# Kernel tuning notes

Measured on AMD Instinct MI355X. Metric: run time of the kernel, lower is better.

The kernel has to match this reference:

```python
import jax, jax.numpy as jnp
import numpy as np

NEG_SLOPE = 0.05

def _leaky(v):
    return jnp.where(v >= 0, v, NEG_SLOPE * v)

def setup_inputs() -> dict:
    key = jax.random.key(0)
    ks = jax.random.split(key, 9)
    B, N, D = 8, 96, 16
    H0, H1, OUT = 50, 50, 64
    x = jax.random.normal(ks[0], (B, N, D), dtype=jnp.float32)
    # dense 0/1 adjacency (float, used directly in matmuls), avg degree ~ 0.15*N
    adj = (jax.random.uniform(ks[1], (B, N, N)) < 0.15).astype(jnp.float32)
    h1 = 3 * D + 3          # 51
    h2 = 2 * D + H0 + 1     # 83
    h3 = D + H1             # 66
    W1 = jax.random.normal(ks[2], (h1, H0), dtype=jnp.float32) / np.sqrt(h1)
    b1 = jax.random.normal(ks[3], (H0,), dtype=jnp.float32) * 0.01
    W2 = jax.random.normal(ks[4], (h2, H1), dtype=jnp.float32) / np.sqrt(h2)
    b2 = jax.random.normal(ks[5], (H1,), dtype=jnp.float32) * 0.01
    W3 = jax.random.normal(ks[6], (h3, OUT), dtype=jnp.float32) / np.sqrt(h3)
    b3 = jax.random.normal(ks[7], (OUT,), dtype=jnp.float32) * 0.01
    return {"x": x, "adj": adj, "W1": W1, "b1": b1, "W2": W2, "b2": b2, "W3": W3, "b3": b3}

def reference(x, adj, W1, b1, W2, b2, W3, b3):
    # Faithful math of SpatialGraphConv.forward, with the O(N^4)/O(N^3)
    # broadcast+concat+GEMM algebraically decomposed into O(N^2) einsums
    # (identical result: the concat-GEMM is a sum of per-block contributions).
    B, N, D = x.shape
    H0 = W1.shape[1]
    # pairwise distances dis[b,i,j]
    diff = x[:, :, None, :] - x[:, None, :, :]            # (B,N,N,D)
    dis = jnp.sqrt(jnp.sum(diff * diff, axis=-1) + 1e-10)  # (B,N,N)
    # split W1 rows per concat block [x_i | x_j | x_k | d_ij | d_jk | d_ik]
    Wxi, Wxj, Wxk = W1[:D], W1[D:2 * D], W1[2 * D:3 * D]
    w_ij, w_jk, w_ik = W1[3 * D], W1[3 * D + 1], W1[3 * D + 2]  # (H0,)
    A = x @ Wxi   # (B,N,H0), indexed by i
    Bm = x @ Wxj  # (B,N,H0), indexed by j
    C = x @ Wxk   # (B,N,H0), indexed by k
    # m3_sum[b,i,j,h] = adj[b,i,j] * sum_k adj[b,j,k] * m3pre[b,i,j,k,h]
    deg = jnp.sum(adj, axis=-1)                           # (B,N): sum_k adj[b,j,k]
    sumC = jnp.einsum('bjk,bkh->bjh', adj, C)             # (B,N,H0)
    sd_jk = jnp.sum(adj * dis, axis=-1)                   # (B,N): sum_k adj[j,k]*dis[j,k]
    sd_ik = jnp.einsum('bik,bjk->bij', dis, adj)          # (B,N,N): sum_k adj[j,k]*dis[i,k]
    S = (deg[:, None, :, None] * (A[:, :, None, :] + Bm[:, None, :, :] + b1
                                   + dis[..., None] * w_ij)
         + sumC[:, None, :, :]
         + sd_jk[:, None, :, None] * w_jk
         + sd_ik[..., None] * w_ik)                        # (B,N,N,H0)
    m3_sum = _leaky(adj[..., None] * S)                    # (B,N,N,H0)
    # stage 2: pairwise concat [x_i | x_j | dis | m3_sum] -> MLP -> adj-masked sum over j
    xi = jnp.broadcast_to(x[:, :, None, :], (B, N, N, D))
    xj = jnp.broadcast_to(x[:, None, :, :], (B, N, N, D))
    feat2 = jnp.concatenate([xi, xj, dis[..., None], m3_sum], axis=-1)  # (B,N,N,2D+1+H0)
    m2 = feat2 @ W2 + b2                                   # (B,N,N,H1)
    m2_sum = _leaky(jnp.einsum('bijh,bij->bih', m2, adj))  # (B,N,H1)
    # stage 3: node-wise MLP
    m1 = _leaky(jnp.concatenate([x, m2_sum], axis=-1) @ W3 + b3)  # (B,N,OUT)
    return m1
```

## Files before the change

### kernel.cpp

```cpp
#include <hip/hip_runtime.h>
#include <math.h>

#define BB   8
#define NN   96
#define DD   16
#define H0D  50
#define H1D  50
#define OUTD 64
#define XP   17

typedef unsigned long long u64;


__device__ __forceinline__ float wave_reduce_sum(float v) {
    #pragma unroll
    for (int off = 1; off < 64; off <<= 1)
        v += __shfl_xor(v, off, 64);
    return v;
}

__global__ __launch_bounds__(64) void kA(
    const float* __restrict__ x, const float* __restrict__ adj,
    const float* __restrict__ W1,
    float* __restrict__ disws, u64* __restrict__ maskws,
    float* __restrict__ degws, float* __restrict__ sdjkws,
    float* __restrict__ nxws, float* __restrict__ APws)
{
    const int b = blockIdx.x / NN, j = blockIdx.x % NN;
    const int lane = threadIdx.x;
    __shared__ float sx[NN * XP];
    __shared__ float snx[DD];

    const float4* x4 = (const float4*)(x + (size_t)b * NN * DD);
    #pragma unroll
    for (int t = lane; t < NN * DD / 4; t += 64) {
        float4 v = x4[t];
        int row = t >> 2, d = (t & 3) * 4;
        float* p = &sx[row * XP + d];
        p[0] = v.x; p[1] = v.y; p[2] = v.z; p[3] = v.w;
    }
    const float* arow = adj + ((size_t)b * NN + j) * NN;
    float a0 = arow[lane];
    float a1 = (lane < NN - 64) ? arow[64 + lane] : 0.f;
    u64 m0 = __ballot(a0 != 0.f);
    u64 m1 = __ballot(a1 != 0.f);
    __syncthreads();

    const float* xj = &sx[j * XP];
    float d0, d1 = 0.f;
    {
        float s = 1e-10f;
        const float* xk = &sx[lane * XP];
        #pragma unroll
        for (int d = 0; d < DD; ++d) { float t = xj[d] - xk[d]; s += t * t; }
        d0 = sqrtf(s);
    }
    if (lane < NN - 64) {
        float s = 1e-10f;
        const float* xk = &sx[(64 + lane) * XP];
        #pragma unroll
        for (int d = 0; d < DD; ++d) { float t = xj[d] - xk[d]; s += t * t; }
        d1 = sqrtf(s);
    }
    float* drow = disws + ((size_t)b * NN + j) * NN;
    drow[lane] = d0;
    if (lane < NN - 64) drow[64 + lane] = d1;

    float deg = (float)(__popcll(m0) + __popcll(m1));
    float part = (((m0 >> lane) & 1) ? d0 : 0.f)
               + ((lane < 32 && ((m1 >> lane) & 1)) ? d1 : 0.f);
    float sdjk = wave_reduce_sum(part);
    if (lane == 0) {
        degws[b * NN + j]  = deg;
        sdjkws[b * NN + j] = sdjk;
        maskws[(b * NN + j) * 2 + 0] = m0;
        maskws[(b * NN + j) * 2 + 1] = m1;
    }

    {
        int c = lane >> 4, d = lane & 15;
        unsigned sm;
        if (c == 0)      sm = (unsigned)(m0 & 0xFFFFFFu);
        else if (c == 1) sm = (unsigned)((m0 >> 24) & 0xFFFFFFu);
        else if (c == 2) sm = (unsigned)((m0 >> 48) & 0xFFFFu) | ((unsigned)(m1 & 0xFFu) << 16);
        else             sm = (unsigned)((m1 >> 8) & 0xFFFFFFu);
        float s = 0.f;
        int base = c * 24;
        while (sm) {
            int k = base + __ffs(sm) - 1;
            sm &= sm - 1;
            s += sx[k * XP + d];
        }
        s += __shfl_xor(s, 16, 64);
        s += __shfl_xor(s, 32, 64);
        if (lane < DD) {
            snx[lane] = s;
            nxws[(b * NN + j) * DD + lane] = s;
        }
    }
    __syncthreads();

    if (lane < H0D) {
        float a = 0.f, bm = 0.f, sc = 0.f;
        #pragma unroll
        for (int d = 0; d < DD; ++d) {
            float xv = xj[d];
            a  += xv * W1[d * H0D + lane];
            bm += xv * W1[(DD + d) * H0D + lane];
            sc += snx[d] * W1[(2 * DD + d) * H0D + lane];
        }
        float* ap = APws + ((size_t)b * NN + j) * 128;
        ap[lane]      = a;
        ap[64 + lane] = deg * bm + sc;
    }
}

__global__ __launch_bounds__(64) void kB(
    const float* __restrict__ x,
    const float* __restrict__ W1, const float* __restrict__ b1,
    const float* __restrict__ W2, const float* __restrict__ b2,
    const float* __restrict__ W3, const float* __restrict__ b3,
    const float* __restrict__ disws, const u64* __restrict__ maskws,
    const float* __restrict__ degws, const float* __restrict__ sdjkws,
    const float* __restrict__ nxws, const float* __restrict__ APws,
    float* __restrict__ out)
{
    const int b = blockIdx.x / NN, i = blockIdx.x % NN;
    const int lane = threadIdx.x;
    __shared__ u64 sm0[NN], sm1[NN];
    __shared__ float sdis[NN], sdeg[NN], ssdjk[NN], ssdik[NN];
    __shared__ float smsum[H0D], sm2[H1D], sxi[DD], snxi[DD];

    const ulonglong2* mp = (const ulonglong2*)(maskws + (size_t)b * NN * 2);
    #pragma unroll
    for (int t = lane; t < NN; t += 64) {
        ulonglong2 m = mp[t];
        sm0[t] = m.x; sm1[t] = m.y;
    }
    const float* drow = disws + ((size_t)b * NN + i) * NN;
    sdis[lane] = drow[lane];
    if (lane < 32) sdis[64 + lane] = drow[64 + lane];
    sdeg[lane] = degws[b * NN + lane];
    if (lane < 32) sdeg[64 + lane] = degws[b * NN + 64 + lane];
    ssdjk[lane] = sdjkws[b * NN + lane];
    if (lane < 32) ssdjk[64 + lane] = sdjkws[b * NN + 64 + lane];
    if (lane < DD) {
        sxi[lane]  = x[((size_t)b * NN + i) * DD + lane];
        snxi[lane] = nxws[(b * NN + i) * DD + lane];
    }
    __syncthreads();

    {
        u64 mm0 = sm0[lane], mm1 = sm1[lane];
        float s = 0.f;
        while (mm0) { int k = __ffsll(mm0) - 1;      mm0 &= mm0 - 1; s += sdis[k]; }
        while (mm1) { int k = 64 + __ffsll(mm1) - 1; mm1 &= mm1 - 1; s += sdis[k]; }
        ssdik[lane] = s;
        if (lane < 32) {
            int j = 64 + lane;
            u64 n0 = sm0[j], n1 = sm1[j];
            float t = 0.f;
            while (n0) { int k = __ffsll(n0) - 1;      n0 &= n0 - 1; t += sdis[k]; }
            while (n1) { int k = 64 + __ffsll(n1) - 1; n1 &= n1 - 1; t += sdis[k]; }
            ssdik[j] = t;
        }
    }
    __syncthreads();

    {
        const int h = (lane < H0D) ? lane : 0;
        float ab  = APws[((size_t)b * NN + i) * 128 + h] + b1[h];
        float wij = W1[(3 * DD + 0) * H0D + h];
        float wjk = W1[(3 * DD + 1) * H0D + h];
        float wik = W1[(3 * DD + 2) * H0D + h];
        float msum = 0.f;
        u64 mm = sm0[i]; int base = 0;
        for (int half = 0; half < 2; ++half) {
            while (mm) {
                int j = base + __ffsll(mm) - 1;
                mm &= mm - 1;
                float S = sdeg[j] * (ab + sdis[j] * wij)
                        + APws[((size_t)b * NN + j) * 128 + 64 + h]
                        + ssdjk[j] * wjk + ssdik[j] * wik;
                msum += (S >= 0.f) ? S : 0.05f * S;
            }
            mm = sm1[i]; base = 64;
        }
        if (lane < H0D) smsum[lane] = msum;
    }
    __syncthreads();

    const float degi = sdeg[i], sdjki = ssdjk[i];
    if (lane < H1D) {
        float s = degi * b2[lane];
        #pragma unroll
        for (int d = 0; d < DD; ++d)
            s += degi * sxi[d] * W2[d * H1D + lane]
               + snxi[d] * W2[(DD + d) * H1D + lane];
        s += sdjki * W2[(2 * DD) * H1D + lane];
        for (int c = 0; c < H0D; ++c)
            s += smsum[c] * W2[(2 * DD + 1 + c) * H1D + lane];
        sm2[lane] = (s >= 0.f) ? s : 0.05f * s;
    }
    __syncthreads();

    {
        float s = b3[lane];
        #pragma unroll
        for (int d = 0; d < DD; ++d) s += sxi[d] * W3[d * OUTD + lane];
        for (int h = 0; h < H1D; ++h) s += sm2[h] * W3[(DD + h) * OUTD + lane];
        s = (s >= 0.f) ? s : 0.05f * s;
        out[((size_t)b * NN + i) * OUTD + lane] = s;
    }
}

extern "C" void kernel_launch(void* const* d_in, const int* in_sizes, int n_in,
                              void* d_out, int out_size, void* d_ws, size_t ws_size,
                              hipStream_t stream) {
    const float* x   = (const float*)d_in[0];
    const float* adj = (const float*)d_in[1];
    const float* W1  = (const float*)d_in[2];
    const float* b1  = (const float*)d_in[3];
    const float* W2  = (const float*)d_in[4];
    const float* b2  = (const float*)d_in[5];
    const float* W3  = (const float*)d_in[6];
    const float* b3  = (const float*)d_in[7];
    float* out = (float*)d_out;

    u64*   maskws = (u64*)d_ws;
    float* fbase  = (float*)((char*)d_ws + BB * NN * 2 * sizeof(u64));
    float* disws  = fbase;
    float* degws  = disws + BB * NN * NN;
    float* sdjkws = degws + BB * NN;
    float* nxws   = sdjkws + BB * NN;
    float* APws   = nxws + BB * NN * DD;

    kA<<<BB * NN, 64, 0, stream>>>(x, adj, W1, disws, maskws, degws, sdjkws, nxws, APws);
    kB<<<BB * NN, 64, 0, stream>>>(x, W1, b1, W2, b2, W3, b3,
                                   disws, maskws, degws, sdjkws, nxws, APws, out);
}
```

Before: 83.96 us.

## Fuse both kernels into one per-node block with recomputed neighbor stats

Replaces the two-kernel pipeline (per-node precompute to global workspace, then per-node aggregation) with a single 256-thread kernel per (batch, node i). Each block recomputes the quantities it needs for each neighbor j (adjacency mask, degree, distance sums, neighbor-feature sums, projected W1 terms), with 4 waves splitting the neighbors. This removes the second launch and the global workspace round trip. The cost is redundant recomputation of per-j data across every block that has j as a neighbor, plus more LDS per block.

```diff
diff --git a/kernel.cpp b/kernel.cpp
--- a/kernel.cpp
+++ b/kernel.cpp
@@ -12,205 +12,204 @@
 typedef unsigned long long u64;
 
 
-__device__ __forceinline__ float wave_reduce_sum(float v) {
-    #pragma unroll
-    for (int off = 1; off < 64; off <<= 1)
-        v += __shfl_xor(v, off, 64);
-    return v;
-}
-
-__global__ __launch_bounds__(64) void kA(
+__global__ __launch_bounds__(256) void sgc_one(
     const float* __restrict__ x, const float* __restrict__ adj,
-    const float* __restrict__ W1,
-    float* __restrict__ disws, u64* __restrict__ maskws,
-    float* __restrict__ degws, float* __restrict__ sdjkws,
-    float* __restrict__ nxws, float* __restrict__ APws)
+    const float* __restrict__ W1, const float* __restrict__ b1,
+    const float* __restrict__ W2, const float* __restrict__ b2,
+    const float* __restrict__ W3, const float* __restrict__ b3,
+    float* __restrict__ out)
 {
-    const int b = blockIdx.x / NN, j = blockIdx.x % NN;
-    const int lane = threadIdx.x;
+    const int b = blockIdx.x / NN, i = blockIdx.x % NN;
+    const int tid = threadIdx.x, wv = tid >> 6, lane = tid & 63;
+
     __shared__ float sx[NN * XP];
-    __shared__ float snx[DD];
+    __shared__ float sdisI[NN];
+    __shared__ int   nbrs[NN];
+    __shared__ int   scnt;
+    __shared__ u64   smi[2];
+    __shared__ float sA[H0D];
+    __shared__ float sP[NN * H0D];
+    __shared__ float sdegc[NN], ssdjkc[NN], ssdikc[NN];
+    __shared__ float pmsum[4 * 64];
+    __shared__ float smsum[H0D];
+    __shared__ float sm2[H1D];
+    __shared__ float snxi[DD];
+    __shared__ float sdegi, ssdjki;
 
     const float4* x4 = (const float4*)(x + (size_t)b * NN * DD);
-    #pragma unroll
-    for (int t = lane; t < NN * DD / 4; t += 64) {
+    for (int t = tid; t < NN * DD / 4; t += 256) {
         float4 v = x4[t];
         int row = t >> 2, d = (t & 3) * 4;
         float* p = &sx[row * XP + d];
         p[0] = v.x; p[1] = v.y; p[2] = v.z; p[3] = v.w;
     }
-    const float* arow = adj + ((size_t)b * NN + j) * NN;
-    float a0 = arow[lane];
-    float a1 = (lane < NN - 64) ? arow[64 + lane] : 0.f;
-    u64 m0 = __ballot(a0 != 0.f);
-    u64 m1 = __ballot(a1 != 0.f);
-    __syncthreads();
-
-    const float* xj = &sx[j * XP];
-    float d0, d1 = 0.f;
+    if (wv == 0) {
+        const float* arow = adj + ((size_t)b * NN + i) * NN;
+        u64 m0 = __ballot(arow[lane] != 0.f);
+        float a1 = (lane < 32) ? arow[64 + lane] : 0.f;
+        u64 m1 = __ballot(a1 != 0.f);
+        int c0 = __popcll(m0);
+        if ((m0 >> lane) & 1)
+            nbrs[__popcll(m0 & ((1ull << lane) - 1))] = lane;
+        if (lane < 32 && ((m1 >> lane) & 1))
+            nbrs[c0 + __popcll(m1 & ((1ull << lane) - 1))] = 64 + lane;
+        if (lane == 0) {
+            int c = c0 + __popcll(m1);
+            scnt = c;
+            smi[0] = m0; smi[1] = m1;
+            sdegi = (float)c;
+        }
+    }
+    __syncthreads();
+
+    if (tid < NN) {
+        const float* xi = &sx[i * XP];
+        const float* xk = &sx[tid * XP];
+        float s = 1e-10f;
+        #pragma unroll
+        for (int d = 0; d < DD; ++d) { float t = xi[d] - xk[d]; s += t * t; }
+        sdisI[tid] = sqrtf(s);
+    } else if (tid < NN + H0D) {
+        int h = tid - NN;
+        float s = 0.f;
+        #pragma unroll
+        for (int d = 0; d < DD; ++d) s += sx[i * XP + d] * W1[d * H0D + h];
+        sA[h] = s;
+    }
+    __syncthreads();
+
+    const int cnt = scnt;
     {
-        float s = 1e-10f;
-        const float* xk = &sx[lane * XP];
-        #pragma unroll
-        for (int d = 0; d < DD; ++d) { float t = xj[d] - xk[d]; s += t * t; }
-        d0 = sqrtf(s);
-    }
-    if (lane < NN - 64) {
-        float s = 1e-10f;
-        const float* xk = &sx[(64 + lane) * XP];
-        #pragma unroll
-        for (int d = 0; d < DD; ++d) { float t = xj[d] - xk[d]; s += t * t; }
-        d1 = sqrtf(s);
-    }
-    float* drow = disws + ((size_t)b * NN + j) * NN;
-    drow[lane] = d0;
-    if (lane < NN - 64) drow[64 + lane] = d1;
-
-    float deg = (float)(__popcll(m0) + __popcll(m1));
-    float part = (((m0 >> lane) & 1) ? d0 : 0.f)
-               + ((lane < 32 && ((m1 >> lane) & 1)) ? d1 : 0.f);
-    float sdjk = wave_reduce_sum(part);
-    if (lane == 0) {
-        degws[b * NN + j]  = deg;
-        sdjkws[b * NN + j] = sdjk;
-        maskws[(b * NN + j) * 2 + 0] = m0;
-        maskws[(b * NN + j) * 2 + 1] = m1;
-    }
+        const int hl = (lane < H0D) ? lane : H0D - 1;
+        float wxj[DD], wxk[DD];
+        #pragma unroll
+        for (int d = 0; d < DD; ++d) {
+            wxj[d] = W1[(DD + d) * H0D + hl];
+            wxk[d] = W1[(2 * DD + d) * H0D + hl];
+        }
+        const int ch = lane >> 4, dd = lane & 15;
+        for (int c = wv; c < cnt; c += 4) {
+            const int j = nbrs[c];
+            const float* arow = adj + ((size_t)b * NN + j) * NN;
+            u64 mj0 = __ballot(arow[lane] != 0.f);
+            float a1 = (lane < 32) ? arow[64 + lane] : 0.f;
+            u64 mj1 = __ballot(a1 != 0.f);
+            float deg = (float)(__popcll(mj0) + __popcll(mj1));
+            const float* xj = &sx[j * XP];
+            float d0, d1 = 0.f;
+            {
+                float s = 1e-10f;
+                const float* xk = &sx[lane * XP];
+                #pragma unroll
+                for (int d = 0; d < DD; ++d) { float t = xj[d] - xk[d]; s += t * t; }
+                d0 = sqrtf(s);
+            }
+            if (lane < 32) {
+                float s = 1e-10f;
+                const float* xk = &sx[(64 + lane) * XP];
+                #pragma unroll
+                for (int d = 0; d < DD; ++d) { float t = xj[d] - xk[d]; s += t * t; }
+                d1 = sqrtf(s);
+            }
+            float p1 = ((mj0 >> lane) & 1) ? d0 : 0.f;
+            float p2 = ((mj0 >> lane) & 1) ? sdisI[lane] : 0.f;
+            if (lane < 32 && ((mj1 >> lane) & 1)) { p1 += d1; p2 += sdisI[64 + lane]; }
+            #pragma unroll
+            for (int off = 1; off < 64; off <<= 1) {
+                p1 += __shfl_xor(p1, off, 64);
+                p2 += __shfl_xor(p2, off, 64);
+            }
+            unsigned sm;
+            if (ch == 0)      sm = (unsigned)(mj0 & 0xFFFFFFu);
+            else if (ch == 1) sm = (unsigned)((mj0 >> 24) & 0xFFFFFFu);
+            else if (ch == 2) sm = (unsigned)((mj0 >> 48) & 0xFFFFu) | ((unsigned)(mj1 & 0xFFu) << 16);
+            else              sm = (unsigned)((mj1 >> 8) & 0xFFFFFFu);
+            float nxv = 0.f;
+            const int base = ch * 24;
+            while (sm) {
+                int k = base + __ffs(sm) - 1;
+                sm &= sm - 1;
+                nxv += sx[k * XP + dd];
+            }
+            nxv += __shfl_xor(nxv, 16, 64);
+            nxv += __shfl_xor(nxv, 32, 64);
+            float bm = 0.f, sc = 0.f;
+            #pragma unroll
+            for (int d = 0; d < DD; ++d) {
+                bm += xj[d] * wxj[d];
+                sc += __shfl(nxv, d, 64) * wxk[d];
+            }
+            if (lane < H0D) sP[c * H0D + lane] = deg * bm + sc;
+            if (lane == 0) { sdegc[c] = deg; ssdjkc[c] = p1; ssdikc[c] = p2; }
+        }
+        if (wv == 0) {
+            u64 mi0 = smi[0], mi1 = smi[1];
+            float p = ((mi0 >> lane) & 1) ? sdisI[lane] : 0.f;
+            if (lane < 32 && ((mi1 >> lane) & 1)) p += sdisI[64 + lane];
+            #pragma unroll
+            for (int off = 1; off < 64; off <<= 1) p += __shfl_xor(p, off, 64);
+            if (lane == 0) ssdjki = p;
+            unsigned sm;
+            if (ch == 0)      sm = (unsigned)(mi0 & 0xFFFFFFu);
+            else if (ch == 1) sm = (unsigned)((mi0 >> 24) & 0xFFFFFFu);
+            else if (ch == 2) sm = (unsigned)((mi0 >> 48) & 0xFFFFu) | ((unsigned)(mi1 & 0xFFu) << 16);
+            else              sm = (unsigned)((mi1 >> 8) & 0xFFFFFFu);
+            float nxv = 0.f;
+            const int base = ch * 24;
+            while (sm) {
+                int k = base + __ffs(sm) - 1;
+                sm &= sm - 1;
+                nxv += sx[k * XP + dd];
+            }
+            nxv += __shfl_xor(nxv, 16, 64);
+            nxv += __shfl_xor(nxv, 32, 64);
+            if (lane < DD) snxi[lane] = nxv;
+        }
+    }
+    __syncthreads();
 
     {
-        int c = lane >> 4, d = lane & 15;
-        unsigned sm;
-        if (c == 0)      sm = (unsigned)(m0 & 0xFFFFFFu);
-        else if (c == 1) sm = (unsigned)((m0 >> 24) & 0xFFFFFFu);
-        else if (c == 2) sm = (unsigned)((m0 >> 48) & 0xFFFFu) | ((unsigned)(m1 & 0xFFu) << 16);
-        else             sm = (unsigned)((m1 >> 8) & 0xFFFFFFu);
-        float s = 0.f;
-        int base = c * 24;
-        while (sm) {
-            int k = base + __ffs(sm) - 1;
-            sm &= sm - 1;
-            s += sx[k * XP + d];
-        }
-        s += __shfl_xor(s, 16, 64);
-        s += __shfl_xor(s, 32, 64);
-        if (lane < DD) {
-            snx[lane] = s;
-            nxws[(b * NN + j) * DD + lane] = s;
-        }
-    }
-    __syncthreads();
-
-    if (lane < H0D) {
-        float a = 0.f, bm = 0.f, sc = 0.f;
-        #pragma unroll
-        for (int d = 0; d < DD; ++d) {
-            float xv = xj[d];
-            a  += xv * W1[d * H0D + lane];
-            bm += xv * W1[(DD + d) * H0D + lane];
-            sc += snx[d] * W1[(2 * DD + d) * H0D + lane];
-        }
-        float* ap = APws + ((size_t)b * NN + j) * 128;
-        ap[lane]      = a;
-        ap[64 + lane] = deg * bm + sc;
-    }
-}
-
-__global__ __launch_bounds__(64) void kB(
-    const float* __restrict__ x,
-    const float* __restrict__ W1, const float* __restrict__ b1,
-    const float* __restrict__ W2, const float* __restrict__ b2,
-    const float* __restrict__ W3, const float* __restrict__ b3,
-    const float* __restrict__ disws, const u64* __restrict__ maskws,
-    const float* __restrict__ degws, const float* __restrict__ sdjkws,
-    const float* __restrict__ nxws, const float* __restrict__ APws,
-    float* __restrict__ out)
-{
-    const int b = blockIdx.x / NN, i = blockIdx.x % NN;
-    const int lane = threadIdx.x;
-    __shared__ u64 sm0[NN], sm1[NN];
-    __shared__ float sdis[NN], sdeg[NN], ssdjk[NN], ssdik[NN];
-    __shared__ float smsum[H0D], sm2[H1D], sxi[DD], snxi[DD];
-
-    const ulonglong2* mp = (const ulonglong2*)(maskws + (size_t)b * NN * 2);
-    #pragma unroll
-    for (int t = lane; t < NN; t += 64) {
-        ulonglong2 m = mp[t];
-        sm0[t] = m.x; sm1[t] = m.y;
-    }
-    const float* drow = disws + ((size_t)b * NN + i) * NN;
-    sdis[lane] = drow[lane];
-    if (lane < 32) sdis[64 + lane] = drow[64 + lane];
-    sdeg[lane] = degws[b * NN + lane];
-    if (lane < 32) sdeg[64 + lane] = degws[b * NN + 64 + lane];
-    ssdjk[lane] = sdjkws[b * NN + lane];
-    if (lane < 32) ssdjk[64 + lane] = sdjkws[b * NN + 64 + lane];
-    if (lane < DD) {
-        sxi[lane]  = x[((size_t)b * NN + i) * DD + lane];
-        snxi[lane] = nxws[(b * NN + i) * DD + lane];
-    }
-    __syncthreads();
-
-    {
-        u64 mm0 = sm0[lane], mm1 = sm1[lane];
-        float s = 0.f;
-        while (mm0) { int k = __ffsll(mm0) - 1;      mm0 &= mm0 - 1; s += sdis[k]; }
-        while (mm1) { int k = 64 + __ffsll(mm1) - 1; mm1 &= mm1 - 1; s += sdis[k]; }
-        ssdik[lane] = s;
-        if (lane < 32) {
-            int j = 64 + lane;
-            u64 n0 = sm0[j], n1 = sm1[j];
-            float t = 0.f;
-            while (n0) { int k = __ffsll(n0) - 1;      n0 &= n0 - 1; t += sdis[k]; }
-            while (n1) { int k = 64 + __ffsll(n1) - 1; n1 &= n1 - 1; t += sdis[k]; }
-            ssdik[j] = t;
-        }
-    }
-    __syncthreads();
-
-    {
-        const int h = (lane < H0D) ? lane : 0;
-        float ab  = APws[((size_t)b * NN + i) * 128 + h] + b1[h];
-        float wij = W1[(3 * DD + 0) * H0D + h];
-        float wjk = W1[(3 * DD + 1) * H0D + h];
-        float wik = W1[(3 * DD + 2) * H0D + h];
+        const int hl = (lane < H0D) ? lane : H0D - 1;
+        float b1v = b1[hl];
+        float wij = W1[(3 * DD + 0) * H0D + hl];
+        float wjk = W1[(3 * DD + 1) * H0D + hl];
+        float wik = W1[(3 * DD + 2) * H0D + hl];
+        float abv = sA[hl] + b1v;
         float msum = 0.f;
-        u64 mm = sm0[i]; int base = 0;
-        for (int half = 0; half < 2; ++half) {
-            while (mm) {
-                int j = base + __ffsll(mm) - 1;
-                mm &= mm - 1;
-                float S = sdeg[j] * (ab + sdis[j] * wij)
-                        + APws[((size_t)b * NN + j) * 128 + 64 + h]
-                        + ssdjk[j] * wjk + ssdik[j] * wik;
-                msum += (S >= 0.f) ? S : 0.05f * S;
-            }
-            mm = sm1[i]; base = 64;
-        }
-        if (lane < H0D) smsum[lane] = msum;
-    }
-    __syncthreads();
-
-    const float degi = sdeg[i], sdjki = ssdjk[i];
-    if (lane < H1D) {
-        float s = degi * b2[lane];
+        for (int c = wv; c < cnt; c += 4) {
+            float S = sdegc[c] * (abv + sdisI[nbrs[c]] * wij)
+                    + sP[c * H0D + hl] + ssdjkc[c] * wjk + ssdikc[c] * wik;
+            msum += (S >= 0.f) ? S : 0.05f * S;
+        }
+        pmsum[wv * 64 + lane] = msum;
+    }
+    __syncthreads();
+
+    if (tid < H0D)
+        smsum[tid] = pmsum[tid] + pmsum[64 + tid] + pmsum[128 + tid] + pmsum[192 + tid];
+    __syncthreads();
+
+    if (tid < H1D) {
+        float dg = sdegi;
+        float s = dg * b2[tid];
         #pragma unroll
         for (int d = 0; d < DD; ++d)
-            s += degi * sxi[d] * W2[d * H1D + lane]
-               + snxi[d] * W2[(DD + d) * H1D + lane];
-        s += sdjki * W2[(2 * DD) * H1D + lane];
+            s += dg * sx[i * XP + d] * W2[d * H1D + tid]
+               + snxi[d] * W2[(DD + d) * H1D + tid];
+        s += ssdjki * W2[(2 * DD) * H1D + tid];
         for (int c = 0; c < H0D; ++c)
-            s += smsum[c] * W2[(2 * DD + 1 + c) * H1D + lane];
-        sm2[lane] = (s >= 0.f) ? s : 0.05f * s;
-    }
-    __syncthreads();
-
-    {
-        float s = b3[lane];
-        #pragma unroll
-        for (int d = 0; d < DD; ++d) s += sxi[d] * W3[d * OUTD + lane];
-        for (int h = 0; h < H1D; ++h) s += sm2[h] * W3[(DD + h) * OUTD + lane];
+            s += smsum[c] * W2[(2 * DD + 1 + c) * H1D + tid];
+        sm2[tid] = (s >= 0.f) ? s : 0.05f * s;
+    }
+    __syncthreads();
+
+    if (tid < OUTD) {
+        float s = b3[tid];
+        #pragma unroll
+        for (int d = 0; d < DD; ++d) s += sx[i * XP + d] * W3[d * OUTD + tid];
+        for (int h = 0; h < H1D; ++h) s += sm2[h] * W3[(DD + h) * OUTD + tid];
         s = (s >= 0.f) ? s : 0.05f * s;
-        out[((size_t)b * NN + i) * OUTD + lane] = s;
+        out[((size_t)b * NN + i) * OUTD + tid] = s;
     }
 }
 
@@ -227,15 +226,5 @@
     const float* b3  = (const float*)d_in[7];
     float* out = (float*)d_out;
 
-    u64*   maskws = (u64*)d_ws;
-    float* fbase  = (float*)((char*)d_ws + BB * NN * 2 * sizeof(u64));
-    float* disws  = fbase;
-    float* degws  = disws + BB * NN * NN;
-    float* sdjkws = degws + BB * NN;
-    float* nxws   = sdjkws + BB * NN;
-    float* APws   = nxws + BB * NN * DD;
-
-    kA<<<BB * NN, 64, 0, stream>>>(x, adj, W1, disws, maskws, degws, sdjkws, nxws, APws);
-    kB<<<BB * NN, 64, 0, stream>>>(x, W1, b1, W2, b2, W3, b3,
-                                   disws, maskws, degws, sdjkws, nxws, APws, out);
+    sgc_one<<<BB * NN, 256, 0, stream>>>(x, adj, W1, b1, W2, b2, W3, b3, out);
 }
```

Result: slower. 85.69 us (+2.1%).
